# Performance work log

Hardware: AMD Instinct MI355X
Metric: run time of the kernel (lower is better)

Reference implementation:

```python
import jax, jax.numpy as jnp
import numpy as np

N_NODES = 100000
N_EDGES = 3200000
N_GRAPHS = 64
F_IN = 16
HID = 64


def gcn_conv(x, W, b, src, dst, ew, n_nodes):
    """PyG GCNConv with add_self_loops=True, symmetric normalization.
    x' = D^{-1/2} (A + I) D^{-1/2} (x W) + b, self-loop weight 1."""
    h = x @ W                                             # [N, out]
    deg = jax.ops.segment_sum(ew, dst, num_segments=n_nodes) + 1.0  # self-loop adds 1
    dinv = jax.lax.rsqrt(jnp.maximum(deg, 1e-12))         # deg_inv_sqrt
    norm = dinv[src] * ew * dinv[dst]                     # [E]
    agg = jax.ops.segment_sum(h[src] * norm[:, None], dst, num_segments=n_nodes)
    agg = agg + h * (dinv * dinv)[:, None]                # self-loop term
    return agg + b


def setup_inputs() -> dict:
    key = jax.random.key(0)
    ks = jax.random.split(key, 12)
    x = jax.random.normal(ks[0], (N_NODES, F_IN), dtype=jnp.float32)
    edge_index = jax.random.randint(ks[1], (2, N_EDGES), 0, N_NODES, dtype=jnp.int64)
    edge_weight = jax.random.uniform(ks[2], (N_EDGES,), dtype=jnp.float32)
    batch = jnp.sort(jax.random.randint(ks[3], (N_NODES,), 0, N_GRAPHS, dtype=jnp.int64))
    # GCN layer params (PyG lin: x @ W with W [in, out])
    s1 = 1.0 / np.sqrt(F_IN)
    s2 = 1.0 / np.sqrt(HID)
    W1 = jax.random.uniform(ks[4], (F_IN, HID), jnp.float32, -s1, s1)
    b1 = jnp.zeros((HID,), jnp.float32)
    W2 = jax.random.uniform(ks[5], (HID, HID), jnp.float32, -s2, s2)
    b2 = jnp.zeros((HID,), jnp.float32)
    W3 = jax.random.uniform(ks[6], (HID, HID), jnp.float32, -s2, s2)
    b3 = jnp.zeros((HID,), jnp.float32)
    Wout = jax.random.uniform(ks[7], (HID, 1), jnp.float32, -s2, s2)
    bout = jax.random.uniform(ks[8], (1,), jnp.float32, -s2, s2)
    return {"x": x, "edge_index": edge_index, "edge_weight": edge_weight,
            "batch": batch, "W1": W1, "b1": b1, "W2": W2, "b2": b2,
            "W3": W3, "b3": b3, "Wout": Wout, "bout": bout}


def reference(x, edge_index, edge_weight, batch, W1, b1, W2, b2, W3, b3, Wout, bout):
    src, dst = edge_index[0], edge_index[1]
    n = x.shape[0]
    # layer 1
    h = gcn_conv(x, W1, b1, src, dst, edge_weight, n)
    # layer 2: sigmoid -> (dropout p=0 identity) -> GCNConv
    h = gcn_conv(jax.nn.sigmoid(h), W2, b2, src, dst, edge_weight, n)
    # layer 3
    h = gcn_conv(jax.nn.sigmoid(h), W3, b3, src, dst, edge_weight, n)
    # global mean pool over graphs
    sums = jax.ops.segment_sum(h, batch, num_segments=N_GRAPHS)          # [G, HID]
    counts = jax.ops.segment_sum(jnp.ones((n,), h.dtype), batch, num_segments=N_GRAPHS)
    pooled = sums / jnp.maximum(counts, 1.0)[:, None]
    # final linear head (dropout p=0 identity)
    return pooled @ Wout + bout                                          # [G, 1]
```

## Files before the change

### kernel.cpp

```cpp
#include <hip/hip_runtime.h>
#include <hip/hip_bf16.h>

#define HID 64
#define P_BLOCKS 1024
#define MAXB 512
#define BCAP 9216
#define TILE 3200
#define NCAP 131072

typedef float v2f __attribute__((ext_vector_type(2)));
typedef unsigned u2v __attribute__((ext_vector_type(2)));

__device__ inline v2f fp8x2_lo(unsigned u) { return __builtin_amdgcn_cvt_pk_f32_fp8(u, false); }
__device__ inline v2f fp8x2_hi(unsigned u) { return __builtin_amdgcn_cvt_pk_f32_fp8(u, true); }

#define GSCALE 16.0f
#define GINV 0.0625f
#define GS1 12.0f
#define GI1 (1.0f / 12.0f)
#define GS2 24.0f
#define GI2 (1.0f / 24.0f)
#define WQINV (1.0f / 4095.0f)

__global__ __launch_bounds__(256) void kp1a_hist(const int* __restrict__ dst,
                                                 int* __restrict__ ghist,
                                                 int nE, int B, int chunk) {
    __shared__ int h[MAXB];
    for (int b = threadIdx.x; b < B; b += 256) h[b] = 0;
    __syncthreads();
    int lo = blockIdx.x * chunk;
    int hi = min(nE, lo + chunk);
    for (int i = lo + threadIdx.x; i < hi; i += 256)
        atomicAdd(&h[dst[i] >> 8], 1);
    __syncthreads();
    for (int b = threadIdx.x; b < B; b += 256)
        ghist[(size_t)b * P_BLOCKS + blockIdx.x] = h[b];
}

__global__ __launch_bounds__(256) void kp1b1_scan(const int* __restrict__ ghist,
                                                  int* __restrict__ goff,
                                                  int* __restrict__ btot) {
    __shared__ int wsum[4];
    __shared__ int woff[4];
    int tid = threadIdx.x;
    int lane = tid & 63, wv = tid >> 6;
    int b = blockIdx.x;
    int4 v = ((const int4*)(ghist + (size_t)b * P_BLOCKS))[tid];
    int s = v.x + v.y + v.z + v.w;
    int sc = s;
#pragma unroll
    for (int off = 1; off < 64; off <<= 1) {
        int t = __shfl_up(sc, off);
        if (lane >= off) sc += t;
    }
    if (lane == 63) wsum[wv] = sc;
    __syncthreads();
    if (tid == 0) {
        int acc = 0;
#pragma unroll
        for (int w = 0; w < 4; ++w) { woff[w] = acc; acc += wsum[w]; }
        btot[b] = acc;
    }
    __syncthreads();
    int ex = woff[wv] + sc - s;
    int4 o;
    o.x = ex;
    o.y = ex + v.x;
    o.z = o.y + v.y;
    o.w = o.z + v.z;
    ((int4*)(goff + (size_t)b * P_BLOCKS))[tid] = o;
}

__global__ __launch_bounds__(512) void kp1b2_scan(const int* __restrict__ btot,
                                                  int* __restrict__ bstart, int B) {
    __shared__ int wsum[8];
    __shared__ int woff[8];
    int tid = threadIdx.x;
    int lane = tid & 63, wv = tid >> 6;
    int tot = (tid < B) ? btot[tid] : 0;
    int sc = tot;
#pragma unroll
    for (int off = 1; off < 64; off <<= 1) {
        int t = __shfl_up(sc, off);
        if (lane >= off) sc += t;
    }
    if (lane == 63) wsum[wv] = sc;
    __syncthreads();
    if (tid == 0) {
        int acc = 0;
#pragma unroll
        for (int w = 0; w < 8; ++w) { woff[w] = acc; acc += wsum[w]; }
        bstart[B] = acc;
    }
    __syncthreads();
    if (tid < B) bstart[tid] = woff[wv] + sc - tot;
}

__global__ __launch_bounds__(256) void kp1c_sort(const int* __restrict__ src,
                                                 const int* __restrict__ dst,
                                                 const float* __restrict__ ew,
                                                 const int* __restrict__ goff,
                                                 const int* __restrict__ bstart,
                                                 int2* __restrict__ bsw,
                                                 int nE, int B, int chunk) {
    __shared__ int2 sorted[TILE];
    __shared__ unsigned short bkt[TILE];
    __shared__ int cnt[MAXB];
    __shared__ int lstart[MAXB];
    __shared__ int lcur[MAXB];
    __shared__ int gcur[MAXB];
    __shared__ int wsum[4];
    __shared__ int woff[4];
    int tid = threadIdx.x;
    int lane = tid & 63, wv = tid >> 6;
    for (int b = tid; b < B; b += 256)
        gcur[b] = bstart[b] + goff[(size_t)b * P_BLOCKS + blockIdx.x];
    int lo = blockIdx.x * chunk;
    int hi = min(nE, lo + chunk);
    for (int tb = lo; tb < hi; tb += TILE) {
        int m = min(hi - tb, TILE);
        cnt[tid] = 0;
        cnt[tid + 256] = 0;
        __syncthreads();
        for (int i = tid; i < m; i += 256)
            atomicAdd(&cnt[dst[tb + i] >> 8], 1);
        __syncthreads();
        int c0 = cnt[2 * tid], c1 = cnt[2 * tid + 1];
        int s = c0 + c1;
        int sc = s;
#pragma unroll
        for (int off = 1; off < 64; off <<= 1) {
            int t = __shfl_up(sc, off);
            if (lane >= off) sc += t;
        }
        if (lane == 63) wsum[wv] = sc;
        __syncthreads();
        if (tid == 0) {
            int acc = 0;
#pragma unroll
            for (int w = 0; w < 4; ++w) { woff[w] = acc; acc += wsum[w]; }
        }
        __syncthreads();
        int ex = woff[wv] + sc - s;
        lstart[2 * tid] = ex;
        lcur[2 * tid] = ex;
        lstart[2 * tid + 1] = ex + c0;
        lcur[2 * tid + 1] = ex + c0;
        __syncthreads();
        for (int i = tid; i < m; i += 256) {
            int d = dst[tb + i];
            int b = d >> 8;
            int pos = atomicAdd(&lcur[b], 1);
            int2 v;
            v.x = src[tb + i] | ((d & 255) << 20);
            v.y = __float_as_int(ew[tb + i]);
            sorted[pos] = v;
            bkt[pos] = (unsigned short)b;
        }
        __syncthreads();
        for (int i = tid; i < m; i += 256) {
            int b = bkt[i];
            bsw[gcur[b] + (i - lstart[b])] = sorted[i];
        }
        __syncthreads();
        for (int b = tid; b < B; b += 256)
            gcur[b] += lcur[b] - lstart[b];
        __syncthreads();
    }
}

__global__ __launch_bounds__(256) void kp2_build(const int2* __restrict__ bsw,
                                                 const int* __restrict__ bstart,
                                                 int* __restrict__ row_start,
                                                 float* __restrict__ dinv,
                                                 unsigned* __restrict__ csr4,
                                                 int n_nodes) {
    __shared__ int2 ebuf[BCAP];
    __shared__ int cnt[256];
    __shared__ float degw[256];
    __shared__ int cur[256];
    __shared__ int wsum[4];
    __shared__ int woff[4];
    int tid = threadIdx.x;
    int lane = tid & 63, wv = tid >> 6;
    int b = blockIdx.x;
    int e0 = bstart[b], e1 = bstart[b + 1];
    int nb = e1 - e0;
    cnt[tid] = 0;
    degw[tid] = 0.0f;
    __syncthreads();
    for (int i = tid; i < nb; i += 256) {
        int2 v = bsw[e0 + i];
        if (i < BCAP) ebuf[i] = v;
        int dlo = (v.x >> 20) & 255;
        atomicAdd(&cnt[dlo], 1);
        atomicAdd(&degw[dlo], __int_as_float(v.y));
    }
    __syncthreads();
    int c = cnt[tid];
    int sc = c;
#pragma unroll
    for (int off = 1; off < 64; off <<= 1) {
        int t = __shfl_up(sc, off);
        if (lane >= off) sc += t;
    }
    if (lane == 63) wsum[wv] = sc;
    __syncthreads();
    if (tid == 0) {
        int acc = 0;
#pragma unroll
        for (int w = 0; w < 4; ++w) { woff[w] = acc; acc += wsum[w]; }
    }
    __syncthreads();
    int ex = woff[wv] + sc - c;
    cur[tid] = ex;
    int node = (b << 8) + tid;
    if (node < n_nodes) {
        row_start[node] = e0 + ex;
        dinv[node] = rsqrtf(fmaxf(degw[tid] + 1.0f, 1e-12f));
    }
    if (b == 0 && tid == 0) row_start[n_nodes] = bstart[gridDim.x];
    __syncthreads();
    for (int i = tid; i < nb; i += 256) {
        int2 v = (i < BCAP) ? ebuf[i] : bsw[e0 + i];
        int dlo = (v.x >> 20) & 255;
        int pos = atomicAdd(&cur[dlo], 1);
        float w = __int_as_float(v.y);
        unsigned wq = (unsigned)(w * 4095.0f + 0.5f);
        csr4[e0 + pos] = ((unsigned)v.x & 0xFFFFFu) | (wq << 20);
    }
}

__global__ __launch_bounds__(256) void k_mm16f4(const float* __restrict__ in,
                                                const float* __restrict__ W,
                                                const float* __restrict__ dinv,
                                                unsigned* __restrict__ gtab,
                                                int n_nodes) {
    __shared__ float Ws[16 * HID];
    for (int i = threadIdx.x; i < 16 * HID; i += 256) Ws[i] = W[i];
    __syncthreads();
    int lane = threadIdx.x & 63;
    int wid = threadIdx.x >> 6;
    int p = lane & 7;
    int q = lane >> 3;
    int nGrp = (n_nodes + 7) >> 3;
    for (int grp = blockIdx.x * 4 + wid; grp < nGrp; grp += gridDim.x * 4) {
        int node = grp * 8 + q;
        bool ok = node < n_nodes;
        float xr0 = ok ? in[node * 16 + p] : 0.0f;
        float xr1 = ok ? in[node * 16 + 8 + p] : 0.0f;
        float di = ok ? dinv[node] : 0.0f;
        v2f a01 = {0.0f, 0.0f}, a23 = {0.0f, 0.0f};
        v2f a45 = {0.0f, 0.0f}, a67 = {0.0f, 0.0f};
#pragma unroll
        for (int k = 0; k < 16; ++k) {
            float xv = __shfl((k < 8) ? xr0 : xr1, q * 8 + (k & 7));
            const float4* wr = (const float4*)&Ws[k * HID + 8 * p];
            float4 w0 = wr[0], w1 = wr[1];
            v2f wl0 = {w0.x, w0.y}, wl1 = {w0.z, w0.w};
            v2f wl2 = {w1.x, w1.y}, wl3 = {w1.z, w1.w};
            a01 += wl0 * xv; a23 += wl1 * xv; a45 += wl2 * xv; a67 += wl3 * xv;
        }
        float sc = di * GS1;
        unsigned pk = __builtin_amdgcn_cvt_scalef32_pk_fp4_f32(0u, a01.x * sc, a01.y * sc, 1.0f, 0);
        pk = __builtin_amdgcn_cvt_scalef32_pk_fp4_f32(pk, a23.x * sc, a23.y * sc, 1.0f, 1);
        pk = __builtin_amdgcn_cvt_scalef32_pk_fp4_f32(pk, a45.x * sc, a45.y * sc, 1.0f, 2);
        pk = __builtin_amdgcn_cvt_scalef32_pk_fp4_f32(pk, a67.x * sc, a67.y * sc, 1.0f, 3);
        if (ok) gtab[(size_t)node * 8 + p] = pk;
    }
}

template <int OUT4>
__global__ __launch_bounds__(256) void k_agg4(const unsigned* __restrict__ g4,
                                              const float* __restrict__ bias,
                                              const float* __restrict__ dinv,
                                              const int* __restrict__ row_start,
                                              const unsigned* __restrict__ csr4,
                                              const float* __restrict__ Wn,
                                              unsigned* __restrict__ outv,
                                              int n_nodes, float ginv_in, float gs_out) {
    int lane = threadIdx.x & 63;
    int wid = threadIdx.x >> 6;
    int node = blockIdx.x * 4 + wid;
    if (node >= n_nodes) return;
    int p = lane & 7;
    int q = lane >> 3;

    float diRaw = dinv[node];

    v2f a01 = {0.0f, 0.0f}, a23 = {0.0f, 0.0f};
    v2f a45 = {0.0f, 0.0f}, a67 = {0.0f, 0.0f};
    {
        unsigned su = g4[(size_t)node * 8 + p];
        if (q == 0) {
            a01 = __builtin_amdgcn_cvt_scalef32_pk_f32_fp4(su, 1.0f, 0);
            a23 = __builtin_amdgcn_cvt_scalef32_pk_f32_fp4(su, 1.0f, 1);
            a45 = __builtin_amdgcn_cvt_scalef32_pk_f32_fp4(su, 1.0f, 2);
            a67 = __builtin_amdgcn_cvt_scalef32_pk_f32_fp4(su, 1.0f, 3);
        }
    }
    int e0 = row_start[node], e1 = row_start[node + 1];
    for (int base = e0; base < e1; base += 64) {
        int m = min(64, e1 - base);
        unsigned sw = 0;
        if (lane < m) sw = __builtin_nontemporal_load(csr4 + base + lane);
        int ng8 = (m + 7) >> 3;
        int ng84 = (ng8 + 3) & ~3;
        for (int g0 = 0; g0 < ng84; g0 += 4) {
            int b8 = 8 * g0 + q;
            unsigned vA = __shfl(sw, b8);
            unsigned vB = __shfl(sw, b8 + 8);
            unsigned vC = __shfl(sw, b8 + 16);
            unsigned vD = __shfl(sw, b8 + 24);
            unsigned uA = g4[(vA & 0xFFFFFu) * 8u + p];
            unsigned uB = g4[(vB & 0xFFFFFu) * 8u + p];
            unsigned uC = g4[(vC & 0xFFFFFu) * 8u + p];
            unsigned uD = g4[(vD & 0xFFFFFu) * 8u + p];
            float wA = (float)(vA >> 20) * WQINV;
            float wB = (float)(vB >> 20) * WQINV;
            float wC = (float)(vC >> 20) * WQINV;
            float wD = (float)(vD >> 20) * WQINV;
            a01 += __builtin_amdgcn_cvt_scalef32_pk_f32_fp4(uA, 1.0f, 0) * wA;
            a23 += __builtin_amdgcn_cvt_scalef32_pk_f32_fp4(uA, 1.0f, 1) * wA;
            a45 += __builtin_amdgcn_cvt_scalef32_pk_f32_fp4(uA, 1.0f, 2) * wA;
            a67 += __builtin_amdgcn_cvt_scalef32_pk_f32_fp4(uA, 1.0f, 3) * wA;
            a01 += __builtin_amdgcn_cvt_scalef32_pk_f32_fp4(uB, 1.0f, 0) * wB;
            a23 += __builtin_amdgcn_cvt_scalef32_pk_f32_fp4(uB, 1.0f, 1) * wB;
            a45 += __builtin_amdgcn_cvt_scalef32_pk_f32_fp4(uB, 1.0f, 2) * wB;
            a67 += __builtin_amdgcn_cvt_scalef32_pk_f32_fp4(uB, 1.0f, 3) * wB;
            a01 += __builtin_amdgcn_cvt_scalef32_pk_f32_fp4(uC, 1.0f, 0) * wC;
            a23 += __builtin_amdgcn_cvt_scalef32_pk_f32_fp4(uC, 1.0f, 1) * wC;
            a45 += __builtin_amdgcn_cvt_scalef32_pk_f32_fp4(uC, 1.0f, 2) * wC;
            a67 += __builtin_amdgcn_cvt_scalef32_pk_f32_fp4(uC, 1.0f, 3) * wC;
            a01 += __builtin_amdgcn_cvt_scalef32_pk_f32_fp4(uD, 1.0f, 0) * wD;
            a23 += __builtin_amdgcn_cvt_scalef32_pk_f32_fp4(uD, 1.0f, 1) * wD;
            a45 += __builtin_amdgcn_cvt_scalef32_pk_f32_fp4(uD, 1.0f, 2) * wD;
            a67 += __builtin_amdgcn_cvt_scalef32_pk_f32_fp4(uD, 1.0f, 3) * wD;
        }
    }
    float a[8] = {a01.x, a01.y, a23.x, a23.y, a45.x, a45.y, a67.x, a67.y};
#pragma unroll
    for (int i = 0; i < 8; ++i) {
        a[i] += __shfl_xor(a[i], 8);
        a[i] += __shfl_xor(a[i], 16);
        a[i] += __shfl_xor(a[i], 32);
    }
    float di = diRaw * ginv_in;
    float4 bv0 = ((const float4*)bias)[2 * p];
    float4 bv1 = ((const float4*)bias)[2 * p + 1];
    a[0] = fmaf(di, a[0], bv0.x); a[1] = fmaf(di, a[1], bv0.y);
    a[2] = fmaf(di, a[2], bv0.z); a[3] = fmaf(di, a[3], bv0.w);
    a[4] = fmaf(di, a[4], bv1.x); a[5] = fmaf(di, a[5], bv1.y);
    a[6] = fmaf(di, a[6], bv1.z); a[7] = fmaf(di, a[7], bv1.w);
    float s[8];
#pragma unroll
    for (int i = 0; i < 8; ++i) s[i] = 1.0f / (1.0f + __expf(-a[i]));
    const float4* Wg = (const float4*)Wn;
    v2f o01 = {0.0f, 0.0f}, o23 = {0.0f, 0.0f};
    v2f o45 = {0.0f, 0.0f}, o67 = {0.0f, 0.0f};
#pragma unroll
    for (int st = 0; st < 8; ++st) {
        float av = __shfl(s[st], q);
        const float4* wr = Wg + ((8 * q + st) * 16 + 2 * p);
        float4 w0 = wr[0], w1 = wr[1];
        v2f wl0 = {w0.x, w0.y}, wl1 = {w0.z, w0.w};
        v2f wl2 = {w1.x, w1.y}, wl3 = {w1.z, w1.w};
        o01 += wl0 * av; o23 += wl1 * av; o45 += wl2 * av; o67 += wl3 * av;
    }
    float o[8] = {o01.x, o01.y, o23.x, o23.y, o45.x, o45.y, o67.x, o67.y};
#pragma unroll
    for (int i = 0; i < 8; ++i) {
        o[i] += __shfl_xor(o[i], 8);
        o[i] += __shfl_xor(o[i], 16);
        o[i] += __shfl_xor(o[i], 32);
    }
    if (lane < 8) {
        float sc = diRaw * gs_out;
        if (OUT4) {
            unsigned pk = __builtin_amdgcn_cvt_scalef32_pk_fp4_f32(0u, o[0] * sc, o[1] * sc, 1.0f, 0);
            pk = __builtin_amdgcn_cvt_scalef32_pk_fp4_f32(pk, o[2] * sc, o[3] * sc, 1.0f, 1);
            pk = __builtin_amdgcn_cvt_scalef32_pk_fp4_f32(pk, o[4] * sc, o[5] * sc, 1.0f, 2);
            pk = __builtin_amdgcn_cvt_scalef32_pk_fp4_f32(pk, o[6] * sc, o[7] * sc, 1.0f, 3);
            __builtin_nontemporal_store(pk, outv + (size_t)node * 8 + p);
        } else {
            unsigned pk0 = __builtin_amdgcn_cvt_pk_fp8_f32(o[0] * sc, o[1] * sc, 0, false);
            pk0 = __builtin_amdgcn_cvt_pk_fp8_f32(o[2] * sc, o[3] * sc, pk0, true);
            unsigned pk1 = __builtin_amdgcn_cvt_pk_fp8_f32(o[4] * sc, o[5] * sc, 0, false);
            pk1 = __builtin_amdgcn_cvt_pk_fp8_f32(o[6] * sc, o[7] * sc, pk1, true);
            u2v pv; pv.x = pk0; pv.y = pk1;
            __builtin_nontemporal_store(pv, ((u2v*)outv) + (size_t)node * 8 + p);
        }
    }
}

__global__ __launch_bounds__(256) void k_dot(const unsigned* __restrict__ g32,
                                             const float* __restrict__ Wout,
                                             const float* __restrict__ b3,
                                             unsigned char* __restrict__ t8,
                                             float* __restrict__ c0,
                                             int n_nodes) {
    __shared__ float Ws[64];
    if (threadIdx.x < 64) Ws[threadIdx.x] = Wout[threadIdx.x];
    __syncthreads();
    int lane = threadIdx.x & 63;
    int wid = threadIdx.x >> 6;
    int p = lane & 15;
    int q = lane >> 4;
    int node = (blockIdx.x * 4 + wid) * 4 + q;
    if (blockIdx.x == 0 && threadIdx.x == 0) {
        float s = 0.0f;
        for (int f = 0; f < 64; ++f) s += b3[f] * Ws[f];
        c0[0] = s;
    }
    if (node >= n_nodes) return;
    unsigned u = g32[(size_t)node * 16 + p];
    v2f lo = fp8x2_lo(u), hi = fp8x2_hi(u);
    float4 wv = ((const float4*)Ws)[p];
    float v = lo.x * wv.x + lo.y * wv.y + hi.x * wv.z + hi.y * wv.w;
    v += __shfl_xor(v, 1);
    v += __shfl_xor(v, 2);
    v += __shfl_xor(v, 4);
    v += __shfl_xor(v, 8);
    if (p == 0) {
        unsigned pk = __builtin_amdgcn_cvt_pk_fp8_f32(v, 0.0f, 0, false);
        t8[node] = (unsigned char)(pk & 0xFFu);
    }
}

__global__ __launch_bounds__(1024) void k_agg3t(const unsigned char* __restrict__ t8,
                                                const int* __restrict__ row_start,
                                                const float* __restrict__ dinv,
                                                const unsigned* __restrict__ csr4,
                                                const float* __restrict__ c0p,
                                                float* __restrict__ p,
                                                int n_nodes, int nbPer) {
    __shared__ unsigned char ts[NCAP];
    int tid = threadIdx.x;
    int ndw = (n_nodes + 3) >> 2;
    const unsigned* t32 = (const unsigned*)t8;
    for (int i = tid; i < ndw; i += 1024) ((unsigned*)ts)[i] = t32[i];
    __syncthreads();
    float c0 = c0p[0];
    int lane = tid & 63, wid = tid >> 6;
    int lo = blockIdx.x * nbPer;
    int hi = min(n_nodes, lo + nbPer);
    for (int node = lo + wid; node < hi; node += 16) {
        int e0 = row_start[node], e1 = row_start[node + 1];
        float acc = 0.0f;
        for (int base = e0; base < e1; base += 64) {
            int i = base + lane;
            unsigned sw = (i < e1) ? csr4[i] : 0u;
            float tv = fp8x2_lo((unsigned)ts[sw & 0xFFFFFu]).x;
            acc += (float)(sw >> 20) * tv;
        }
        acc *= WQINV;
#pragma unroll
        for (int off = 32; off; off >>= 1) acc += __shfl_xor(acc, off);
        if (lane == 0) {
            float self = fp8x2_lo((unsigned)ts[node]).x;
            p[node] = fmaf(dinv[node] * GINV, acc + self, c0);
        }
    }
}

__global__ __launch_bounds__(256) void k_poolseg(const float* __restrict__ p,
                                                 const int* __restrict__ batch,
                                                 float* __restrict__ psum,
                                                 float* __restrict__ pcnt,
                                                 int n_nodes) {
    int lane = threadIdx.x & 63;
    int gw = (blockIdx.x * blockDim.x + threadIdx.x) >> 6;
    int node = gw * 64 + lane;
    bool valid = node < n_nodes;
    float v = valid ? p[node] : 0.0f;
    int g = valid ? batch[node] : -1;
    int g0 = __shfl(g, 0);
    if (__all((g == g0) && valid)) {
#pragma unroll
        for (int off = 32; off; off >>= 1) v += __shfl_xor(v, off);
        if (lane == 0) {
            atomicAdd(&psum[g0], v);
            atomicAdd(&pcnt[g0], 64.0f);
        }
    } else if (valid) {
        atomicAdd(&psum[g], v);
        atomicAdd(&pcnt[g], 1.0f);
    }
}

__global__ __launch_bounds__(64) void k_out(const float* __restrict__ psum,
                                            const float* __restrict__ pcnt,
                                            const float* __restrict__ bout,
                                            float* __restrict__ out, int G) {
    int g = threadIdx.x;
    if (g < G) out[g] = psum[g] / fmaxf(pcnt[g], 1.0f) + bout[0];
}

extern "C" void kernel_launch(void* const* d_in, const int* in_sizes, int n_in,
                              void* d_out, int out_size, void* d_ws, size_t ws_size,
                              hipStream_t stream) {
    const float* x    = (const float*)d_in[0];
    const int*   eidx = (const int*)d_in[1];
    const float* ew   = (const float*)d_in[2];
    const int*   batch= (const int*)d_in[3];
    const float* W1   = (const float*)d_in[4];
    const float* b1   = (const float*)d_in[5];
    const float* W2   = (const float*)d_in[6];
    const float* b2   = (const float*)d_in[7];
    const float* W3   = (const float*)d_in[8];
    const float* b3   = (const float*)d_in[9];
    const float* Wout = (const float*)d_in[10];
    const float* bout = (const float*)d_in[11];
    float* out = (float*)d_out;

    const int N = in_sizes[0] / 16;
    const int E = in_sizes[2];
    const int G = out_size;
    const int* src = eidx;
    const int* dst = eidx + E;
    const int B = (N + 255) >> 8;
    const int chunk = (E + P_BLOCKS - 1) / P_BLOCKS;

    size_t off = 0;
    auto carve = [&](size_t bytes) -> void* {
        void* p = (char*)d_ws + off;
        off += (bytes + 255) & ~(size_t)255;
        return p;
    };
    float* psum     = (float*)carve(64 * 4);
    float* pcnt     = (float*)carve(64 * 4);
    size_t zero_bytes = off;
    int*   ghist    = (int*)  carve((size_t)B * P_BLOCKS * 4);
    int*   goff     = (int*)  carve((size_t)B * P_BLOCKS * 4);
    int*   btot     = (int*)  carve((size_t)B * 4);
    int*   bstart   = (int*)  carve((size_t)(B + 1) * 4);
    int2*  bsw      = (int2*) carve((size_t)E * 8);
    int*   row_start= (int*)  carve((size_t)(N + 1) * 4);
    unsigned* csr4  = (unsigned*)carve((size_t)E * 4);
    float* dinv     = (float*)carve((size_t)N * 4);
    unsigned* gA    = (unsigned*)carve((size_t)N * HID);
    unsigned* gB    = (unsigned*)carve((size_t)N * HID);
    float* p        = (float*)carve((size_t)N * 4);
    unsigned char* t8 = (unsigned char*)carve((size_t)N + 256);
    float* c0buf    = (float*)carve(256);
    (void)ws_size;

    (void)hipMemsetAsync(d_ws, 0, zero_bytes, stream);

    const int nodeBlocks = (N + 3) / 4;
    const int waveBlocks = ((N + 63) / 64 * 64 + 255) / 256;
    const int mmB4 = (((N + 7) >> 3) + 3) / 4;

    kp1a_hist<<<P_BLOCKS, 256, 0, stream>>>(dst, ghist, E, B, chunk);
    kp1b1_scan<<<B, 256, 0, stream>>>(ghist, goff, btot);
    kp1b2_scan<<<1, 512, 0, stream>>>(btot, bstart, B);
    kp1c_sort<<<P_BLOCKS, 256, 0, stream>>>(src, dst, ew, goff, bstart,
                                            bsw, E, B, chunk);
    kp2_build<<<B, 256, 0, stream>>>(bsw, bstart, row_start, dinv, csr4, N);

    k_mm16f4<<<mmB4, 256, 0, stream>>>(x, W1, dinv, gA, N);
    k_agg4<1><<<nodeBlocks, 256, 0, stream>>>(gA, b1, dinv, row_start, csr4,
                                              W2, gB, N, GI1, GS2);
    k_agg4<0><<<nodeBlocks, 256, 0, stream>>>(gB, b2, dinv, row_start, csr4,
                                              W3, gA, N, GI2, GSCALE);
    k_dot<<<(N + 15) / 16, 256, 0, stream>>>(gA, Wout, b3, t8, c0buf, N);
    k_agg3t<<<256, 1024, 0, stream>>>(t8, row_start, dinv, csr4, c0buf, p, N,
                                      (N + 255) / 256);

    k_poolseg<<<waveBlocks, 256, 0, stream>>>(p, batch, psum, pcnt, N);
    k_out<<<1, 64, 0, stream>>>(psum, pcnt, bout, out, G);
}
```

Baseline: 425.1 us.

## Fold W3·Wout into layer-2 aggregation and drop separate dot kernel

Precomputes W3·Wout as a 64-vector in a tiny kernel, so the second aggregation kernel emits one fp8 scalar per node instead of a 64-wide fp8 row. This removes the k_dot pass and the 64-byte-per-node intermediate write and read. The final aggregation switches from a 1024-thread LDS-staged kernel to a one-wave-per-node kernel that reads the byte table straight from global memory. The risk is that these global gathers are less local than the previous LDS reads.

```diff
diff --git a/kernel.cpp b/kernel.cpp
--- a/kernel.cpp
+++ b/kernel.cpp
@@ -6,10 +6,8 @@
 #define MAXB 512
 #define BCAP 9216
 #define TILE 3200
-#define NCAP 131072
 
 typedef float v2f __attribute__((ext_vector_type(2)));
-typedef unsigned u2v __attribute__((ext_vector_type(2)));
 
 __device__ inline v2f fp8x2_lo(unsigned u) { return __builtin_amdgcn_cvt_pk_f32_fp8(u, false); }
 __device__ inline v2f fp8x2_hi(unsigned u) { return __builtin_amdgcn_cvt_pk_f32_fp8(u, true); }
@@ -231,6 +229,22 @@
     }
 }
 
+__global__ __launch_bounds__(64) void k_wtilde(const float* __restrict__ W3,
+                                               const float* __restrict__ Wout,
+                                               const float* __restrict__ b3,
+                                               float* __restrict__ wtil,
+                                               float* __restrict__ c0) {
+    int j = threadIdx.x;
+    float s = 0.0f;
+    for (int k = 0; k < 64; ++k) s += W3[j * 64 + k] * Wout[k];
+    wtil[j] = s;
+    if (j == 0) {
+        float c = 0.0f;
+        for (int k = 0; k < 64; ++k) c += b3[k] * Wout[k];
+        c0[0] = c;
+    }
+}
+
 __global__ __launch_bounds__(256) void k_mm16f4(const float* __restrict__ in,
                                                 const float* __restrict__ W,
                                                 const float* __restrict__ dinv,
@@ -277,7 +291,7 @@
                                               const int* __restrict__ row_start,
                                               const unsigned* __restrict__ csr4,
                                               const float* __restrict__ Wn,
-                                              unsigned* __restrict__ outv,
+                                              void* __restrict__ outv,
                                               int n_nodes, float ginv_in, float gs_out) {
     int lane = threadIdx.x & 63;
     int wid = threadIdx.x >> 6;
@@ -355,111 +369,75 @@
     float s[8];
 #pragma unroll
     for (int i = 0; i < 8; ++i) s[i] = 1.0f / (1.0f + __expf(-a[i]));
-    const float4* Wg = (const float4*)Wn;
-    v2f o01 = {0.0f, 0.0f}, o23 = {0.0f, 0.0f};
-    v2f o45 = {0.0f, 0.0f}, o67 = {0.0f, 0.0f};
-#pragma unroll
-    for (int st = 0; st < 8; ++st) {
-        float av = __shfl(s[st], q);
-        const float4* wr = Wg + ((8 * q + st) * 16 + 2 * p);
-        float4 w0 = wr[0], w1 = wr[1];
-        v2f wl0 = {w0.x, w0.y}, wl1 = {w0.z, w0.w};
-        v2f wl2 = {w1.x, w1.y}, wl3 = {w1.z, w1.w};
-        o01 += wl0 * av; o23 += wl1 * av; o45 += wl2 * av; o67 += wl3 * av;
-    }
-    float o[8] = {o01.x, o01.y, o23.x, o23.y, o45.x, o45.y, o67.x, o67.y};
-#pragma unroll
-    for (int i = 0; i < 8; ++i) {
-        o[i] += __shfl_xor(o[i], 8);
-        o[i] += __shfl_xor(o[i], 16);
-        o[i] += __shfl_xor(o[i], 32);
-    }
-    if (lane < 8) {
-        float sc = diRaw * gs_out;
-        if (OUT4) {
+
+    if (OUT4) {
+        const float4* Wg = (const float4*)Wn;
+        v2f o01 = {0.0f, 0.0f}, o23 = {0.0f, 0.0f};
+        v2f o45 = {0.0f, 0.0f}, o67 = {0.0f, 0.0f};
+#pragma unroll
+        for (int st = 0; st < 8; ++st) {
+            float av = __shfl(s[st], q);
+            const float4* wr = Wg + ((8 * q + st) * 16 + 2 * p);
+            float4 w0 = wr[0], w1 = wr[1];
+            v2f wl0 = {w0.x, w0.y}, wl1 = {w0.z, w0.w};
+            v2f wl2 = {w1.x, w1.y}, wl3 = {w1.z, w1.w};
+            o01 += wl0 * av; o23 += wl1 * av; o45 += wl2 * av; o67 += wl3 * av;
+        }
+        float o[8] = {o01.x, o01.y, o23.x, o23.y, o45.x, o45.y, o67.x, o67.y};
+#pragma unroll
+        for (int i = 0; i < 8; ++i) {
+            o[i] += __shfl_xor(o[i], 8);
+            o[i] += __shfl_xor(o[i], 16);
+            o[i] += __shfl_xor(o[i], 32);
+        }
+        if (lane < 8) {
+            float sc = diRaw * gs_out;
             unsigned pk = __builtin_amdgcn_cvt_scalef32_pk_fp4_f32(0u, o[0] * sc, o[1] * sc, 1.0f, 0);
             pk = __builtin_amdgcn_cvt_scalef32_pk_fp4_f32(pk, o[2] * sc, o[3] * sc, 1.0f, 1);
             pk = __builtin_amdgcn_cvt_scalef32_pk_fp4_f32(pk, o[4] * sc, o[5] * sc, 1.0f, 2);
             pk = __builtin_amdgcn_cvt_scalef32_pk_fp4_f32(pk, o[6] * sc, o[7] * sc, 1.0f, 3);
-            __builtin_nontemporal_store(pk, outv + (size_t)node * 8 + p);
-        } else {
-            unsigned pk0 = __builtin_amdgcn_cvt_pk_fp8_f32(o[0] * sc, o[1] * sc, 0, false);
-            pk0 = __builtin_amdgcn_cvt_pk_fp8_f32(o[2] * sc, o[3] * sc, pk0, true);
-            unsigned pk1 = __builtin_amdgcn_cvt_pk_fp8_f32(o[4] * sc, o[5] * sc, 0, false);
-            pk1 = __builtin_amdgcn_cvt_pk_fp8_f32(o[6] * sc, o[7] * sc, pk1, true);
-            u2v pv; pv.x = pk0; pv.y = pk1;
-            __builtin_nontemporal_store(pv, ((u2v*)outv) + (size_t)node * 8 + p);
-        }
-    }
-}
-
-__global__ __launch_bounds__(256) void k_dot(const unsigned* __restrict__ g32,
-                                             const float* __restrict__ Wout,
-                                             const float* __restrict__ b3,
-                                             unsigned char* __restrict__ t8,
-                                             float* __restrict__ c0,
-                                             int n_nodes) {
-    __shared__ float Ws[64];
-    if (threadIdx.x < 64) Ws[threadIdx.x] = Wout[threadIdx.x];
-    __syncthreads();
+            __builtin_nontemporal_store(pk, (unsigned*)outv + (size_t)node * 8 + p);
+        }
+    } else {
+        const float4* wt4 = (const float4*)Wn;
+        float4 w0 = wt4[2 * p], w1 = wt4[2 * p + 1];
+        float local = s[0] * w0.x + s[1] * w0.y + s[2] * w0.z + s[3] * w0.w
+                    + s[4] * w1.x + s[5] * w1.y + s[6] * w1.z + s[7] * w1.w;
+        local += __shfl_xor(local, 1);
+        local += __shfl_xor(local, 2);
+        local += __shfl_xor(local, 4);
+        if (lane == 0) {
+            unsigned pk = __builtin_amdgcn_cvt_pk_fp8_f32(local * diRaw * gs_out, 0.0f, 0, false);
+            ((unsigned char*)outv)[node] = (unsigned char)(pk & 0xFFu);
+        }
+    }
+}
+
+__global__ __launch_bounds__(256) void k_agg3s(const unsigned char* __restrict__ t8,
+                                               const int* __restrict__ row_start,
+                                               const float* __restrict__ dinv,
+                                               const unsigned* __restrict__ csr4,
+                                               const float* __restrict__ c0p,
+                                               float* __restrict__ p,
+                                               int n_nodes) {
     int lane = threadIdx.x & 63;
     int wid = threadIdx.x >> 6;
-    int p = lane & 15;
-    int q = lane >> 4;
-    int node = (blockIdx.x * 4 + wid) * 4 + q;
-    if (blockIdx.x == 0 && threadIdx.x == 0) {
-        float s = 0.0f;
-        for (int f = 0; f < 64; ++f) s += b3[f] * Ws[f];
-        c0[0] = s;
-    }
+    int node = blockIdx.x * 4 + wid;
     if (node >= n_nodes) return;
-    unsigned u = g32[(size_t)node * 16 + p];
-    v2f lo = fp8x2_lo(u), hi = fp8x2_hi(u);
-    float4 wv = ((const float4*)Ws)[p];
-    float v = lo.x * wv.x + lo.y * wv.y + hi.x * wv.z + hi.y * wv.w;
-    v += __shfl_xor(v, 1);
-    v += __shfl_xor(v, 2);
-    v += __shfl_xor(v, 4);
-    v += __shfl_xor(v, 8);
-    if (p == 0) {
-        unsigned pk = __builtin_amdgcn_cvt_pk_fp8_f32(v, 0.0f, 0, false);
-        t8[node] = (unsigned char)(pk & 0xFFu);
-    }
-}
-
-__global__ __launch_bounds__(1024) void k_agg3t(const unsigned char* __restrict__ t8,
-                                                const int* __restrict__ row_start,
-                                                const float* __restrict__ dinv,
-                                                const unsigned* __restrict__ csr4,
-                                                const float* __restrict__ c0p,
-                                                float* __restrict__ p,
-                                                int n_nodes, int nbPer) {
-    __shared__ unsigned char ts[NCAP];
-    int tid = threadIdx.x;
-    int ndw = (n_nodes + 3) >> 2;
-    const unsigned* t32 = (const unsigned*)t8;
-    for (int i = tid; i < ndw; i += 1024) ((unsigned*)ts)[i] = t32[i];
-    __syncthreads();
-    float c0 = c0p[0];
-    int lane = tid & 63, wid = tid >> 6;
-    int lo = blockIdx.x * nbPer;
-    int hi = min(n_nodes, lo + nbPer);
-    for (int node = lo + wid; node < hi; node += 16) {
-        int e0 = row_start[node], e1 = row_start[node + 1];
-        float acc = 0.0f;
-        for (int base = e0; base < e1; base += 64) {
-            int i = base + lane;
-            unsigned sw = (i < e1) ? csr4[i] : 0u;
-            float tv = fp8x2_lo((unsigned)ts[sw & 0xFFFFFu]).x;
-            acc += (float)(sw >> 20) * tv;
-        }
-        acc *= WQINV;
-#pragma unroll
-        for (int off = 32; off; off >>= 1) acc += __shfl_xor(acc, off);
-        if (lane == 0) {
-            float self = fp8x2_lo((unsigned)ts[node]).x;
-            p[node] = fmaf(dinv[node] * GINV, acc + self, c0);
-        }
+    int e0 = row_start[node], e1 = row_start[node + 1];
+    float acc = 0.0f;
+    for (int base = e0; base < e1; base += 64) {
+        int i = base + lane;
+        unsigned sw = (i < e1) ? __builtin_nontemporal_load(csr4 + i) : 0u;
+        float tv = fp8x2_lo((unsigned)t8[sw & 0xFFFFFu]).x;
+        acc += (float)(sw >> 20) * tv;
+    }
+    acc *= WQINV;
+#pragma unroll
+    for (int off = 32; off; off >>= 1) acc += __shfl_xor(acc, off);
+    if (lane == 0) {
+        float self = fp8x2_lo((unsigned)t8[node]).x;
+        p[node] = fmaf(dinv[node] * GINV, acc + self, c0p[0]);
     }
 }
 
@@ -532,7 +510,7 @@
     size_t zero_bytes = off;
     int*   ghist    = (int*)  carve((size_t)B * P_BLOCKS * 4);
     int*   goff     = (int*)  carve((size_t)B * P_BLOCKS * 4);
-    int*   btot     = (int*)  carve((size_t)B * 4);
+    int*   btot    = (int*)  carve((size_t)B * 4);
     int*   bstart   = (int*)  carve((size_t)(B + 1) * 4);
     int2*  bsw      = (int2*) carve((size_t)E * 8);
     int*   row_start= (int*)  carve((size_t)(N + 1) * 4);
@@ -543,6 +521,7 @@
     float* p        = (float*)carve((size_t)N * 4);
     unsigned char* t8 = (unsigned char*)carve((size_t)N + 256);
     float* c0buf    = (float*)carve(256);
+    float* wtil     = (float*)carve(64 * 4);
     (void)ws_size;
 
     (void)hipMemsetAsync(d_ws, 0, zero_bytes, stream);
@@ -550,6 +529,8 @@
     const int nodeBlocks = (N + 3) / 4;
     const int waveBlocks = ((N + 63) / 64 * 64 + 255) / 256;
     const int mmB4 = (((N + 7) >> 3) + 3) / 4;
+
+    k_wtilde<<<1, 64, 0, stream>>>(W3, Wout, b3, wtil, c0buf);
 
     kp1a_hist<<<P_BLOCKS, 256, 0, stream>>>(dst, ghist, E, B, chunk);
     kp1b1_scan<<<B, 256, 0, stream>>>(ghist, goff, btot);
@@ -560,12 +541,11 @@
 
     k_mm16f4<<<mmB4, 256, 0, stream>>>(x, W1, dinv, gA, N);
     k_agg4<1><<<nodeBlocks, 256, 0, stream>>>(gA, b1, dinv, row_start, csr4,
-                                              W2, gB, N, GI1, GS2);
+                                              W2, (void*)gB, N, GI1, GS2);
     k_agg4<0><<<nodeBlocks, 256, 0, stream>>>(gB, b2, dinv, row_start, csr4,
-                                              W3, gA, N, GI2, GSCALE);
-    k_dot<<<(N + 15) / 16, 256, 0, stream>>>(gA, Wout, b3, t8, c0buf, N);
-    k_agg3t<<<256, 1024, 0, stream>>>(t8, row_start, dinv, csr4, c0buf, p, N,
-                                      (N + 255) / 256);
+                                              wtil, (void*)t8, N, GI2, GSCALE);
+    k_agg3s<<<nodeBlocks, 256, 0, stream>>>(t8, row_start, dinv, csr4, c0buf,
+                                            p, N);
 
     k_poolseg<<<waveBlocks, 256, 0, stream>>>(p, batch, psum, pcnt, N);
     k_out<<<1, 64, 0, stream>>>(psum, pcnt, bout, out, G);
```

Measured after the change: 391.5 us. 7.9% less time.
